# Kernel optimization log

Hardware: AMD Instinct MI355X
Metric: run time of the kernel (lower is better)

## Reference

```python
import jax, jax.numpy as jnp
import numpy as np

N_SAMPLES = 16384
SR = 22050.0
B = 8
N_OSC = 128
TWO_PI = 2.0 * np.pi


def setup_inputs() -> dict:
    key = jax.random.key(0)
    k1, k2, k3, k4 = jax.random.split(key, 4)
    centers = jnp.asarray(np.geomspace(20.0, 10000.0, N_OSC), dtype=jnp.float32)
    bandwidths = 0.108 * centers + 24.7  # erb(f)
    freq_params = jax.random.uniform(k1, (B, N_OSC, 64), jnp.float32, -10.0, 10.0)
    amp_params = jax.random.uniform(k2, (B, N_OSC, 64), jnp.float32, 0.0, 0.01)
    noise_params = jax.random.uniform(k3, (B, 17, 1024), jnp.float32, 0.0, 0.01)
    noise = jax.random.uniform(k4, (B, N_SAMPLES), jnp.float32, -1.0, 1.0)
    return {
        'freq_params': freq_params,
        'amp_params': amp_params,
        'noise_params': noise_params,
        'centers': centers,
        'bandwidths': bandwidths,
        'noise': noise,
    }


def linear_upsample(x, out_size):
    # F.upsample(mode='linear', align_corners=False) on last dim
    in_size = x.shape[-1]
    scale = in_size / out_size
    coords = (jnp.arange(out_size, dtype=jnp.float32) + 0.5) * scale - 0.5
    coords = jnp.clip(coords, 0.0, in_size - 1)
    lo = jnp.floor(coords).astype(jnp.int32)
    hi = jnp.minimum(lo + 1, in_size - 1)
    w = coords - lo.astype(jnp.float32)
    return x[..., lo] * (1.0 - w) + x[..., hi] * w


def oscillator_bank(frequency, amplitude, sample_rate):
    # frequency, amplitude: (batch, n_osc, n_samples)
    frequency = jnp.clip(frequency, 1.0, sample_rate / 2.0)
    omegas = frequency * (TWO_PI / sample_rate)
    phases = jnp.cumsum(omegas, axis=-1)  # phase accumulation (prefix scan)
    return jnp.sum(jnp.cos(phases) * amplitude, axis=1)  # (batch, n_samples)


def noise_bank2(x, noise):
    # x: (b, n_coeffs=17, n_frames=1024) filter magnitudes; noise: (b, total_samples)
    b, mags, frames = x.shape
    win = (mags - 1) * 2  # 32
    hop = win // 2        # 16
    total = hop * frames  # 16384
    npad = jnp.pad(noise, ((0, 0), (0, hop)))
    idx = jnp.arange(frames)[:, None] * hop + jnp.arange(win)[None, :]
    nf = npad[:, idx]
    coeffs = jnp.fft.rfft(nf, norm='ortho')            # (b, frames, mags) complex
    filtered = coeffs * jnp.transpose(x, (0, 2, 1))    # per-frame spectral shaping
    wav = jnp.fft.irfft(filtered, n=win, norm='ortho')
    a = wav[..., :hop]
    c = wav[..., hop:]
    c = jnp.concatenate([jnp.zeros_like(c[:, :1]), c[:, :-1]], axis=1)
    return (a + c).reshape(b, 1, total)


def reference(freq_params, amp_params, noise_params, centers, bandwidths, noise):
    orig_freq = jnp.tanh(freq_params)                                   # (B,128,64)
    freq = centers[None, :, None] + orig_freq * (bandwidths[None, :, None] / 2.0)
    orig_amp = jax.nn.relu(amp_params)                                  # (B,128,64)
    noisep = jax.nn.relu(noise_params)                                  # (B,17,1024)
    freq_up = linear_upsample(freq, N_SAMPLES)                          # (B,128,16384)
    amp_up = linear_upsample(orig_amp, N_SAMPLES)                       # (B,128,16384)
    x = oscillator_bank(freq_up, amp_up, SR)                            # (B,16384)
    n = noise_bank2(noisep, noise)                                      # (B,1,16384)
    x = x.reshape(n.shape)
    return (x + n, orig_freq, orig_amp, x, n)
```

## Files before the change

kernel.cpp:

```cpp
#include <hip/hip_runtime.h>
#include <hip/hip_bf16.h>
#include <math.h>

#define NS    16384
#define NOSC  128
#define NCTRL 64
#define NB    8

#define OFF_SUM 0
#define OFF_OF  131072
#define OFF_OA  196608
#define OFF_X   262144
#define OFF_N   393216

#define OMEGA_SC 2.8495170054464554e-4f

__device__ __forceinline__ bool looks_like_freq(const float* __restrict__ A)
{
    float mx = 0.0f;
#pragma unroll
    for (int j = 0; j < 8; ++j) mx = fmaxf(mx, fabsf(A[j]));
    return mx > 0.02f;
}

__global__ __launch_bounds__(256) void k_prep(const float* __restrict__ pA,
                                              const float* __restrict__ pB,
                                              const float* __restrict__ cA,
                                              const float* __restrict__ cB,
                                              float* __restrict__ wsW,
                                              float* __restrict__ wsP,
                                              float* __restrict__ out)
{
    const bool Afreq = looks_like_freq(pA);
    const float* fp = Afreq ? pA : pB;
    const float* ap = Afreq ? pB : pA;
    const bool AisC = (cA[0] < 23.0f);
    const float* centers = AisC ? cA : cB;
    const float* bws     = AisC ? cB : cA;

    const int wid  = (blockIdx.x * 256 + threadIdx.x) >> 6;
    const int lane = threadIdx.x & 63;
    const int osc  = wid & (NOSC - 1);

    const float fv = fp[wid * NCTRL + lane];
    const float av = ap[wid * NCTRL + lane];
    const float of = tanhf(fv);
    out[OFF_OF + wid * NCTRL + lane] = of;
    out[OFF_OA + wid * NCTRL + lane] = fmaxf(av, 0.0f);

    float fr = fmaf(of, 0.5f * bws[osc], centers[osc]);
    fr = fminf(fmaxf(fr, 1.0f), 11025.0f);
    const float wk = fr * OMEGA_SC;
    wsW[lane * 1024 + wid] = wk;

    const float wkm1 = __shfl_up(wk, 1, 64);
    double s = (lane == 0) ? 128.0 * (double)wk
                           : 128.0 * ((double)wkm1 + (double)wk);
#pragma unroll
    for (int d = 1; d < 64; d <<= 1) {
        double t = __shfl_up(s, d, 64);
        if (lane >= d) s += t;
    }
    const double TWOPI  = 6.283185307179586;
    const double INV2PI = 0.15915494309189535;
    wsP[lane * 1024 + wid] = (float)(s - TWOPI * rint(s * INV2PI));
}

__global__ __launch_bounds__(256) void k_osc(const float* __restrict__ pA,
                                             const float* __restrict__ pB,
                                             const float* __restrict__ wsW,
                                             const float* __restrict__ wsP,
                                             float* __restrict__ out)
{
    const bool Afreq = looks_like_freq(pA);
    const float* ap = Afreq ? pB : pA;

    const int T = blockIdx.x;
    const int b = blockIdx.y;
    const int tid = threadIdx.x;

    __shared__ float4 sQ[2][NOSC];
    __shared__ float  sD[2][NOSC];

    if (tid < NOSC) {
        const int gid = b * NOSC + tid;
        const int cm1 = (T == 0) ? 0 : T - 1;
        const int cp1 = (T == 63) ? 63 : T + 1;
        float w_m1 = wsW[cm1 * 1024 + gid];
        float w_0  = wsW[T   * 1024 + gid];
        float w_p1 = wsW[cp1 * 1024 + gid];
        float P_m1 = (T == 0) ? 0.0f : wsP[(T - 1) * 1024 + gid];
        float P_0  = wsP[T * 1024 + gid];
        if (T == 0) w_m1 = w_0;

        const float* a = ap + gid * NCTRL;
        float a_m1 = fmaxf(a[cm1], 0.0f);
        float a_0  = fmaxf(a[T],   0.0f);
        float a_p1 = fmaxf(a[cp1], 0.0f);

        sQ[0][tid] = make_float4(w_m1, w_0 - w_m1, P_m1, a_m1);
        sD[0][tid] = a_0 - a_m1;
        sQ[1][tid] = make_float4(w_0, w_p1 - w_0, P_0, a_0);
        sD[1][tid] = a_p1 - a_0;
    }
    __syncthreads();

    const int hi = tid >> 7;
    const int r  = hi ? (tid - 128) : (tid + 128);
    float r1 = (float)(r + 1);
    if (T == 0 && hi == 0) r1 = (float)(tid + 1);
    const float r2 = (float)((r + 1) * (r + 1)) * (1.0f / 512.0f);
    const float fr = ((float)r + 0.5f) * (1.0f / 256.0f);

    float acc0 = 0.0f, acc1 = 0.0f, acc2 = 0.0f, acc3 = 0.0f;
#pragma unroll 4
    for (int o = 0; o < NOSC; o += 4) {
        float4 q0 = sQ[hi][o + 0];
        float4 q1 = sQ[hi][o + 1];
        float4 q2 = sQ[hi][o + 2];
        float4 q3 = sQ[hi][o + 3];
        float p0 = fmaf(r2, q0.y, fmaf(r1, q0.x, q0.z));
        float p1 = fmaf(r2, q1.y, fmaf(r1, q1.x, q1.z));
        float p2 = fmaf(r2, q2.y, fmaf(r1, q2.x, q2.z));
        float p3 = fmaf(r2, q3.y, fmaf(r1, q3.x, q3.z));
        float m0 = fmaf(fr, sD[hi][o + 0], q0.w);
        float m1 = fmaf(fr, sD[hi][o + 1], q1.w);
        float m2 = fmaf(fr, sD[hi][o + 2], q2.w);
        float m3 = fmaf(fr, sD[hi][o + 3], q3.w);
        acc0 = fmaf(__cosf(p0), m0, acc0);
        acc1 = fmaf(__cosf(p1), m1, acc1);
        acc2 = fmaf(__cosf(p2), m2, acc2);
        acc3 = fmaf(__cosf(p3), m3, acc3);
    }
    out[OFF_X + b * NS + T * 256 + tid] = (acc0 + acc1) + (acc2 + acc3);
}

__global__ __launch_bounds__(256) void k_osc_fb(const float* __restrict__ pA,
                                                const float* __restrict__ pB,
                                                const float* __restrict__ cA,
                                                const float* __restrict__ cB,
                                                float* __restrict__ out)
{
    const bool Afreq = looks_like_freq(pA);
    const float* fp = Afreq ? pA : pB;
    const float* ap = Afreq ? pB : pA;
    const bool AisC = (cA[0] < 23.0f);
    const float* centers = AisC ? cA : cB;
    const float* bws     = AisC ? cB : cA;

    const int T = blockIdx.x, b = blockIdx.y, tid = threadIdx.x;
    __shared__ float4 sQ[2][NOSC];
    __shared__ float  sD[2][NOSC];

    if (tid < NOSC) {
        const int gid = b * NOSC + tid;
        const int cm1 = (T == 0) ? 0 : T - 1;
        const int cp1 = (T == 63) ? 63 : T + 1;
        const float ctr = centers[tid];
        const float hbw = 0.5f * bws[tid];
        const float* f = fp + gid * NCTRL;
        const double TWOPI  = 6.283185307179586;
        const double INV2PI = 0.15915494309189535;
        double P = 0.0;
        float wprev = 0.0f, w_m1 = 0.0f, w_0 = 0.0f, w_p1 = 0.0f;
        float P_m1 = 0.0f, P_0 = 0.0f;
        const int kmax = (T == 63) ? 63 : T + 1;
        for (int k = 0; k <= kmax; ++k) {
            float of = tanhf(f[k]);
            float fr2 = fminf(fmaxf(fmaf(of, hbw, ctr), 1.0f), 11025.0f);
            float wk = fr2 * OMEGA_SC;
            if (k == 0) P = 128.0 * (double)wk;
            else        P += 128.0 * ((double)wprev + (double)wk);
            if (k == T - 1) { w_m1 = wk; P_m1 = (float)(P - TWOPI * rint(P * INV2PI)); }
            if (k == T)     { w_0  = wk; P_0  = (float)(P - TWOPI * rint(P * INV2PI)); }
            if (k == kmax)  { w_p1 = wk; }
            wprev = wk;
        }
        if (T == 0) { w_m1 = w_0; P_m1 = 0.0f; }
        const float* a = ap + gid * NCTRL;
        float a_m1 = fmaxf(a[cm1], 0.0f);
        float a_0  = fmaxf(a[T],   0.0f);
        float a_p1 = fmaxf(a[cp1], 0.0f);
        sQ[0][tid] = make_float4(w_m1, w_0 - w_m1, P_m1, a_m1);
        sD[0][tid] = a_0 - a_m1;
        sQ[1][tid] = make_float4(w_0, w_p1 - w_0, P_0, a_0);
        sD[1][tid] = a_p1 - a_0;
    }
    __syncthreads();

    const int hi = tid >> 7;
    const int r  = hi ? (tid - 128) : (tid + 128);
    float r1 = (float)(r + 1);
    if (T == 0 && hi == 0) r1 = (float)(tid + 1);
    const float r2 = (float)((r + 1) * (r + 1)) * (1.0f / 512.0f);
    const float fr = ((float)r + 0.5f) * (1.0f / 256.0f);

    float acc = 0.0f;
#pragma unroll 4
    for (int o = 0; o < NOSC; ++o) {
        float4 q = sQ[hi][o];
        float ph = fmaf(r1, q.x, q.z);
        ph       = fmaf(r2, q.y, ph);
        float amp = fmaf(fr, sD[hi][o], q.w);
        acc = fmaf(__cosf(ph), amp, acc);
    }
    out[OFF_X + b * NS + T * 256 + tid] = acc;
}

__global__ __launch_bounds__(256) void k_params(const float* __restrict__ pA,
                                                const float* __restrict__ pB,
                                                float* __restrict__ out)
{
    const bool Afreq = looks_like_freq(pA);
    const float* fp = Afreq ? pA : pB;
    const float* ap = Afreq ? pB : pA;
    int i = blockIdx.x * 256 + threadIdx.x;
    if (i < NB * NOSC * NCTRL) {
        out[OFF_OF + i] = tanhf(fp[i]);
        out[OFF_OA + i] = fmaxf(ap[i], 0.0f);
    }
}

__global__ __launch_bounds__(544) void k_noise(const float* __restrict__ nparams,
                                               const float* __restrict__ noise,
                                               float* __restrict__ out)
{
    __shared__ float nf[288];
    __shared__ float cosT[32], sinT[32];
    __shared__ float Rm[17][18], Sm[17][18];
    __shared__ float y[17][32];

    const int tid = threadIdx.x;
    const int b   = blockIdx.y;
    const int F0  = blockIdx.x * 16;
    const int fi  = tid >> 5;
    const int t   = tid & 31;
    const int f   = F0 + fi - 1;

    if (tid < 32) {
        float th = (float)tid * 0.19634954084936207f;
        cosT[tid] = cosf(th);
        sinT[tid] = sinf(th);
    }
    const int sbase = (F0 - 1) * 16;
    for (int j = tid; j < 288; j += 544) {
        int gidx = sbase + j;
        nf[j] = (gidx >= 0 && gidx < NS) ? noise[b * NS + gidx] : 0.0f;
    }
    __syncthreads();

    if (t < 17) {
        const int k = t;
        float re = 0.0f, im = 0.0f;
        const int s0 = fi * 16;
#pragma unroll
        for (int s = 0; s < 32; ++s) {
            float v = nf[s0 + s];
            int j = (k * s) & 31;
            re = fmaf(v, cosT[j], re);
            im = fmaf(v, sinT[j], im);
        }
        float m = (f >= 0) ? fmaxf(nparams[(b * 17 + k) * 1024 + f], 0.0f) : 0.0f;
        Rm[fi][k] = re * m;
        Sm[fi][k] = im * m;
    }
    __syncthreads();

    {
        float a = Rm[fi][0];
#pragma unroll
        for (int k = 1; k <= 15; ++k) {
            int j = (k * t) & 31;
            a = fmaf(2.0f * Rm[fi][k], cosT[j], a);
            a = fmaf(2.0f * Sm[fi][k], sinT[j], a);
        }
        a += (t & 1) ? -Rm[fi][16] : Rm[fi][16];
        y[fi][t] = a * 0.03125f;
    }
    __syncthreads();

    if (fi >= 1 && t < 16) {
        const int base = b * NS + f * 16 + t;
        float nv = y[fi][t] + y[fi - 1][16 + t];
        out[OFF_N + base] = nv;
        out[OFF_SUM + base] = out[OFF_X + base] + nv;
    }
}

extern "C" void kernel_launch(void* const* d_in, const int* in_sizes, int n_in,
                              void* d_out, int out_size, void* d_ws, size_t ws_size,
                              hipStream_t stream)
{
    const float* s65536[2] = {nullptr, nullptr}; int n65 = 0;
    const float* s128[2]   = {nullptr, nullptr}; int n12 = 0;
    const float* nparams = nullptr;
    const float* noise   = nullptr;
    for (int i = 0; i < n_in; ++i) {
        const float* p = (const float*)d_in[i];
        switch (in_sizes[i]) {
            case 65536:  if (n65 < 2) s65536[n65++] = p; break;
            case 128:    if (n12 < 2) s128[n12++]   = p; break;
            case 139264: nparams = p; break;
            case 131072: noise   = p; break;
            default: break;
        }
    }
    float* out = (float*)d_out;

    if (ws_size >= 2u * 65536u * sizeof(float)) {
        float* wsW = (float*)d_ws;
        float* wsP = wsW + 65536;
        k_prep<<<256, 256, 0, stream>>>(s65536[0], s65536[1], s128[0], s128[1],
                                        wsW, wsP, out);
        k_osc<<<dim3(64, 8), 256, 0, stream>>>(s65536[0], s65536[1], wsW, wsP, out);
    } else {
        k_params<<<256, 256, 0, stream>>>(s65536[0], s65536[1], out);
        k_osc_fb<<<dim3(64, 8), 256, 0, stream>>>(s65536[0], s65536[1],
                                                  s128[0], s128[1], out);
    }
    k_noise<<<dim3(64, 8), 544, 0, stream>>>(nparams, noise, out);
}
```

Before: 79.99 us.

## Fuse noise filterbank into oscillator kernel and precompute per-segment coefficients

The prep kernel now writes packed per-segment records (omega, delta-omega, phase, amp, delta-amp) in 32-byte entries, so the oscillator loop reads wave-uniform coefficients straight from global memory instead of staging them through shared memory. The noise DFT/filter/inverse-DFT overlap-add is merged into the oscillator kernel, which removes one launch and writes the sum output directly. In exchange, each block does the noise work with 256 threads instead of 544, and the workspace grows.

New measurement: 90.22 us. 1.13x slower.

```diff
diff --git a/kernel.cpp b/kernel.cpp
--- a/kernel.cpp
+++ b/kernel.cpp
@@ -1,5 +1,4 @@
 #include <hip/hip_runtime.h>
-#include <hip/hip_bf16.h>
 #include <math.h>
 
 #define NS    16384
@@ -15,6 +14,8 @@
 
 #define OMEGA_SC 2.8495170054464554e-4f
 
+#define SEG_FLOATS ((size_t)NB * 65 * NOSC * 8)
+
 __device__ __forceinline__ bool looks_like_freq(const float* __restrict__ A)
 {
     float mx = 0.0f;
@@ -27,8 +28,7 @@
                                               const float* __restrict__ pB,
                                               const float* __restrict__ cA,
                                               const float* __restrict__ cB,
-                                              float* __restrict__ wsW,
-                                              float* __restrict__ wsP,
+                                              float* __restrict__ segs,
                                               float* __restrict__ out)
 {
     const bool Afreq = looks_like_freq(pA);
@@ -41,17 +41,18 @@
     const int wid  = (blockIdx.x * 256 + threadIdx.x) >> 6;
     const int lane = threadIdx.x & 63;
     const int osc  = wid & (NOSC - 1);
+    const int b    = wid >> 7;
 
     const float fv = fp[wid * NCTRL + lane];
     const float av = ap[wid * NCTRL + lane];
     const float of = tanhf(fv);
+    const float ar = fmaxf(av, 0.0f);
     out[OFF_OF + wid * NCTRL + lane] = of;
-    out[OFF_OA + wid * NCTRL + lane] = fmaxf(av, 0.0f);
+    out[OFF_OA + wid * NCTRL + lane] = ar;
 
     float fr = fmaf(of, 0.5f * bws[osc], centers[osc]);
     fr = fminf(fmaxf(fr, 1.0f), 11025.0f);
     const float wk = fr * OMEGA_SC;
-    wsW[lane * 1024 + wid] = wk;
 
     const float wkm1 = __shfl_up(wk, 1, 64);
     double s = (lane == 0) ? 128.0 * (double)wk
@@ -63,45 +64,79 @@
     }
     const double TWOPI  = 6.283185307179586;
     const double INV2PI = 0.15915494309189535;
-    wsP[lane * 1024 + wid] = (float)(s - TWOPI * rint(s * INV2PI));
-}
-
-__global__ __launch_bounds__(256) void k_osc(const float* __restrict__ pA,
-                                             const float* __restrict__ pB,
-                                             const float* __restrict__ wsW,
-                                             const float* __restrict__ wsP,
-                                             float* __restrict__ out)
-{
-    const bool Afreq = looks_like_freq(pA);
-    const float* ap = Afreq ? pB : pA;
-
+    const float Pk = (float)(s - TWOPI * rint(s * INV2PI));
+
+    const float wk1 = __shfl_down(wk, 1, 64);
+    const float ak1 = __shfl_down(ar, 1, 64);
+    const float dw = (lane == 63) ? 0.0f : wk1 - wk;
+    const float da = (lane == 63) ? 0.0f : ak1 - ar;
+
+    float* e = segs + (((size_t)b * 65 + (lane + 1)) * NOSC + osc) * 8;
+    *(float4*)e       = make_float4(wk, dw, Pk, ar);
+    *(float4*)(e + 4) = make_float4(da, 0.0f, 0.0f, 0.0f);
+    if (lane == 0) {
+        float* h = segs + ((size_t)b * 65 * NOSC + osc) * 8;
+        *(float4*)h       = make_float4(wk, 0.0f, 0.0f, ar);
+        *(float4*)(h + 4) = make_float4(0.0f, 0.0f, 0.0f, 0.0f);
+    }
+}
+
+__global__ __launch_bounds__(256) void k_fused(const float* __restrict__ segs,
+                                               const float* __restrict__ nparams,
+                                               const float* __restrict__ noise,
+                                               float* __restrict__ out)
+{
     const int T = blockIdx.x;
     const int b = blockIdx.y;
     const int tid = threadIdx.x;
 
-    __shared__ float4 sQ[2][NOSC];
-    __shared__ float  sD[2][NOSC];
-
-    if (tid < NOSC) {
-        const int gid = b * NOSC + tid;
-        const int cm1 = (T == 0) ? 0 : T - 1;
-        const int cp1 = (T == 63) ? 63 : T + 1;
-        float w_m1 = wsW[cm1 * 1024 + gid];
-        float w_0  = wsW[T   * 1024 + gid];
-        float w_p1 = wsW[cp1 * 1024 + gid];
-        float P_m1 = (T == 0) ? 0.0f : wsP[(T - 1) * 1024 + gid];
-        float P_0  = wsP[T * 1024 + gid];
-        if (T == 0) w_m1 = w_0;
-
-        const float* a = ap + gid * NCTRL;
-        float a_m1 = fmaxf(a[cm1], 0.0f);
-        float a_0  = fmaxf(a[T],   0.0f);
-        float a_p1 = fmaxf(a[cp1], 0.0f);
-
-        sQ[0][tid] = make_float4(w_m1, w_0 - w_m1, P_m1, a_m1);
-        sD[0][tid] = a_0 - a_m1;
-        sQ[1][tid] = make_float4(w_0, w_p1 - w_0, P_0, a_0);
-        sD[1][tid] = a_p1 - a_0;
+    __shared__ float nf[288];
+    __shared__ float cosT[32], sinT[32];
+    __shared__ float Rm[17][18], Sm[17][18];
+    __shared__ float y[17][33];
+
+    if (tid < 32) {
+        float th = (float)tid * 0.19634954084936207f;
+        cosT[tid] = cosf(th);
+        sinT[tid] = sinf(th);
+    }
+    const int sbase = T * 256 - 16;
+    for (int j = tid; j < 288; j += 256) {
+        int g = sbase + j;
+        nf[j] = (g >= 0 && g < NS) ? noise[b * NS + g] : 0.0f;
+    }
+    __syncthreads();
+
+    for (int w = tid; w < 289; w += 256) {
+        int fi = (int)(((unsigned)w * 0x0F0F1u) >> 20);
+        int k  = w - fi * 17;
+        int f  = T * 16 + fi - 1;
+        float re = 0.0f, im = 0.0f;
+        const int s0 = fi * 16;
+#pragma unroll
+        for (int s = 0; s < 32; ++s) {
+            float v = nf[s0 + s];
+            int j = (k * s) & 31;
+            re = fmaf(v, cosT[j], re);
+            im = fmaf(v, sinT[j], im);
+        }
+        float m = (f >= 0) ? fmaxf(nparams[(b * 17 + k) * 1024 + f], 0.0f) : 0.0f;
+        Rm[fi][k] = re * m;
+        Sm[fi][k] = im * m;
+    }
+    __syncthreads();
+
+    for (int w = tid; w < 544; w += 256) {
+        int fi = w >> 5, t = w & 31;
+        float a = Rm[fi][0];
+#pragma unroll
+        for (int k = 1; k <= 15; ++k) {
+            int j = (k * t) & 31;
+            a = fmaf(2.0f * Rm[fi][k], cosT[j], a);
+            a = fmaf(2.0f * Sm[fi][k], sinT[j], a);
+        }
+        a += (t & 1) ? -Rm[fi][16] : Rm[fi][16];
+        y[fi][t] = a * 0.03125f;
     }
     __syncthreads();
 
@@ -112,27 +147,51 @@
     const float r2 = (float)((r + 1) * (r + 1)) * (1.0f / 512.0f);
     const float fr = ((float)r + 0.5f) * (1.0f / 256.0f);
 
+    const int soff = __builtin_amdgcn_readfirstlane(((b * 65 + T + hi) * NOSC) * 8);
+    const float* __restrict__ sp = segs + soff;
+
     float acc0 = 0.0f, acc1 = 0.0f, acc2 = 0.0f, acc3 = 0.0f;
 #pragma unroll 4
     for (int o = 0; o < NOSC; o += 4) {
-        float4 q0 = sQ[hi][o + 0];
-        float4 q1 = sQ[hi][o + 1];
-        float4 q2 = sQ[hi][o + 2];
-        float4 q3 = sQ[hi][o + 3];
-        float p0 = fmaf(r2, q0.y, fmaf(r1, q0.x, q0.z));
-        float p1 = fmaf(r2, q1.y, fmaf(r1, q1.x, q1.z));
-        float p2 = fmaf(r2, q2.y, fmaf(r1, q2.x, q2.z));
-        float p3 = fmaf(r2, q3.y, fmaf(r1, q3.x, q3.z));
-        float m0 = fmaf(fr, sD[hi][o + 0], q0.w);
-        float m1 = fmaf(fr, sD[hi][o + 1], q1.w);
-        float m2 = fmaf(fr, sD[hi][o + 2], q2.w);
-        float m3 = fmaf(fr, sD[hi][o + 3], q3.w);
+        const float* e0 = sp + ((o + 0) << 3);
+        const float* e1 = sp + ((o + 1) << 3);
+        const float* e2 = sp + ((o + 2) << 3);
+        const float* e3 = sp + ((o + 3) << 3);
+        float p0 = fmaf(r2, e0[1], fmaf(r1, e0[0], e0[2]));
+        float p1 = fmaf(r2, e1[1], fmaf(r1, e1[0], e1[2]));
+        float p2 = fmaf(r2, e2[1], fmaf(r1, e2[0], e2[2]));
+        float p3 = fmaf(r2, e3[1], fmaf(r1, e3[0], e3[2]));
+        float m0 = fmaf(fr, e0[4], e0[3]);
+        float m1 = fmaf(fr, e1[4], e1[3]);
+        float m2 = fmaf(fr, e2[4], e2[3]);
+        float m3 = fmaf(fr, e3[4], e3[3]);
         acc0 = fmaf(__cosf(p0), m0, acc0);
         acc1 = fmaf(__cosf(p1), m1, acc1);
         acc2 = fmaf(__cosf(p2), m2, acc2);
         acc3 = fmaf(__cosf(p3), m3, acc3);
     }
-    out[OFF_X + b * NS + T * 256 + tid] = (acc0 + acc1) + (acc2 + acc3);
+    const float xv = (acc0 + acc1) + (acc2 + acc3);
+
+    const int fo = tid >> 4, u = tid & 15;
+    const float nv = y[fo + 1][u] + y[fo][16 + u];
+    const int base = b * NS + T * 256 + tid;
+    out[OFF_X   + base] = xv;
+    out[OFF_N   + base] = nv;
+    out[OFF_SUM + base] = xv + nv;
+}
+
+__global__ __launch_bounds__(256) void k_params(const float* __restrict__ pA,
+                                                const float* __restrict__ pB,
+                                                float* __restrict__ out)
+{
+    const bool Afreq = looks_like_freq(pA);
+    const float* fp = Afreq ? pA : pB;
+    const float* ap = Afreq ? pB : pA;
+    int i = blockIdx.x * 256 + threadIdx.x;
+    if (i < NB * NOSC * NCTRL) {
+        out[OFF_OF + i] = tanhf(fp[i]);
+        out[OFF_OA + i] = fmaxf(ap[i], 0.0f);
+    }
 }
 
 __global__ __launch_bounds__(256) void k_osc_fb(const float* __restrict__ pA,
@@ -207,23 +266,9 @@
     out[OFF_X + b * NS + T * 256 + tid] = acc;
 }
 
-__global__ __launch_bounds__(256) void k_params(const float* __restrict__ pA,
-                                                const float* __restrict__ pB,
-                                                float* __restrict__ out)
-{
-    const bool Afreq = looks_like_freq(pA);
-    const float* fp = Afreq ? pA : pB;
-    const float* ap = Afreq ? pB : pA;
-    int i = blockIdx.x * 256 + threadIdx.x;
-    if (i < NB * NOSC * NCTRL) {
-        out[OFF_OF + i] = tanhf(fp[i]);
-        out[OFF_OA + i] = fmaxf(ap[i], 0.0f);
-    }
-}
-
-__global__ __launch_bounds__(544) void k_noise(const float* __restrict__ nparams,
-                                               const float* __restrict__ noise,
-                                               float* __restrict__ out)
+__global__ __launch_bounds__(544) void k_noise_fb(const float* __restrict__ nparams,
+                                                  const float* __restrict__ noise,
+                                                  float* __restrict__ out)
 {
     __shared__ float nf[288];
     __shared__ float cosT[32], sinT[32];
@@ -307,16 +352,15 @@
     }
     float* out = (float*)d_out;
 
-    if (ws_size >= 2u * 65536u * sizeof(float)) {
-        float* wsW = (float*)d_ws;
-        float* wsP = wsW + 65536;
+    if (ws_size >= SEG_FLOATS * sizeof(float)) {
+        float* segs = (float*)d_ws;
         k_prep<<<256, 256, 0, stream>>>(s65536[0], s65536[1], s128[0], s128[1],
-                                        wsW, wsP, out);
-        k_osc<<<dim3(64, 8), 256, 0, stream>>>(s65536[0], s65536[1], wsW, wsP, out);
+                                        segs, out);
+        k_fused<<<dim3(64, 8), 256, 0, stream>>>(segs, nparams, noise, out);
     } else {
         k_params<<<256, 256, 0, stream>>>(s65536[0], s65536[1], out);
         k_osc_fb<<<dim3(64, 8), 256, 0, stream>>>(s65536[0], s65536[1],
                                                   s128[0], s128[1], out);
-    }
-    k_noise<<<dim3(64, 8), 544, 0, stream>>>(nparams, noise, out);
-}
+        k_noise_fb<<<dim3(64, 8), 544, 0, stream>>>(nparams, noise, out);
+    }
+}
```
